# Kernel optimization log

Hardware: AMD Instinct MI355X
Metric: run time of the kernel (lower is better)

Reference implementation:

```python
import jax, jax.numpy as jnp
import numpy as np

B, S, H, U = 32, 2048, 1024, 1024


def setup_inputs() -> dict:
    key = jax.random.key(0)
    ks = jax.random.split(key, 8)
    sH = 1.0 / np.sqrt(H)
    sU = 1.0 / np.sqrt(U)
    return {
        "encoder_output": jax.random.normal(ks[0], (B, S, H), dtype=jnp.float32),
        "last_layer_h_n": jax.random.normal(ks[1], (B, H), dtype=jnp.float32),
        # torch Linear stores weight [out,in]; we store transposed [in,out] for x @ W
        "W1_w": jax.random.uniform(ks[2], (H, U), jnp.float32, -sH, sH),
        "W1_b": jax.random.uniform(ks[3], (U,), jnp.float32, -sH, sH),
        "W2_w": jax.random.uniform(ks[4], (H, U), jnp.float32, -sH, sH),
        "W2_b": jax.random.uniform(ks[5], (U,), jnp.float32, -sH, sH),
        "V_w": jax.random.uniform(ks[6], (U, 1), jnp.float32, -sU, sU),
        "V_b": jax.random.uniform(ks[7], (1,), jnp.float32, -sU, sU),
    }


def reference(encoder_output, last_layer_h_n, W1_w, W1_b, W2_w, W2_b, V_w, V_b):
    # proj_enc: [B,S,U]; proj_h: [B,1,U] (unsqueeze(1) broadcast)
    proj_enc = jnp.einsum("bsh,hu->bsu", encoder_output, W1_w) + W1_b
    proj_h = (last_layer_h_n @ W2_w + W2_b)[:, None, :]
    # score: [B,S,1]
    score = jnp.tanh(proj_enc + proj_h) @ V_w + V_b
    # softmax over the sequence axis (dim 1)
    attention_weights = jax.nn.softmax(score, axis=1)
    # NOTE: in the original module context_vector is always None (dead branch),
    # so the faithful output is attention_weights alone.
    return attention_weights
```

## Files before the change

### kernel.cpp

```cpp
#include <hip/hip_runtime.h>
#include <hip/hip_bf16.h>


typedef __bf16 bf16x8 __attribute__((ext_vector_type(8)));
typedef float  f32x4  __attribute__((ext_vector_type(4)));

#define HDIM 1024
#define UDIM 1024
#define SDIM 2048
#define MROWS 65536
#define BM 128
#define BN 128
#define BK 32

__device__ inline unsigned short f2bf(float x) {
    return __builtin_bit_cast(unsigned short, (__bf16)x);
}

__device__ inline float fast_tanh(float x) {
    float z = __expf(-2.0f * __builtin_fabsf(x));
    float t = __fdividef(1.0f - z, 1.0f + z);
    return __builtin_copysignf(t, x);
}

#define GLDS16(gp, lp)                                                              \
    __builtin_amdgcn_global_load_lds(                                               \
        (const __attribute__((address_space(1))) unsigned int*)(gp),                \
        (__attribute__((address_space(3))) unsigned int*)(lp), 16, 0, 0)

__global__ __launch_bounds__(256) void cvt_kernel(const float* __restrict__ in,
                                                  unsigned short* __restrict__ out) {
    size_t i = ((size_t)blockIdx.x * 256 + threadIdx.x) * 8;
    const float4 f0 = *(const float4*)(in + i);
    const float4 f1 = *(const float4*)(in + i + 4);
    ushort4 h0, h1;
    h0.x = f2bf(f0.x); h0.y = f2bf(f0.y); h0.z = f2bf(f0.z); h0.w = f2bf(f0.w);
    h1.x = f2bf(f1.x); h1.y = f2bf(f1.y); h1.z = f2bf(f1.z); h1.w = f2bf(f1.w);
    *(ushort4*)(out + i) = h0;
    *(ushort4*)(out + i + 4) = h1;
}

__global__ void w1t_kernel(const float* __restrict__ W1, unsigned short* __restrict__ W1T) {
    __shared__ float tile[32][33];
    int bx = blockIdx.x;
    int by = blockIdx.y;
    int tx = threadIdx.x, ty = threadIdx.y;
#pragma unroll
    for (int r = 0; r < 4; ++r) {
        int h = by * 32 + ty + r * 8;
        int u = bx * 32 + tx;
        tile[ty + r * 8][tx] = W1[h * UDIM + u];
    }
    __syncthreads();
#pragma unroll
    for (int r = 0; r < 4; ++r) {
        int u = bx * 32 + ty + r * 8;
        int h = by * 32 + tx;
        W1T[u * HDIM + h] = f2bf(tile[tx][ty + r * 8]);
    }
}

__global__ void php_kernel(const float* __restrict__ hn, const float* __restrict__ W2,
                           float* __restrict__ php) {
    int u = (blockIdx.x & 3) * 256 + threadIdx.x;
    int b = blockIdx.y;
    int hc = blockIdx.z;
    int h0 = hc * 128;
    float acc = 0.f;
#pragma unroll 8
    for (int h = h0; h < h0 + 128; ++h)
        acc = fmaf(hn[b * HDIM + h], W2[h * UDIM + u], acc);
    php[(hc * 32 + b) * UDIM + u] = acc;
}

__global__ void ph_combine(const float* __restrict__ php, const float* __restrict__ W1b,
                           const float* __restrict__ W2b, float* __restrict__ ph) {
    int idx = blockIdx.x * 256 + threadIdx.x;
    int u = idx & (UDIM - 1);
    int b = idx >> 10;
    float acc = W1b[u] + W2b[u];
#pragma unroll
    for (int p = 0; p < 8; ++p) acc += php[(p * 32 + b) * UDIM + u];
    ph[idx] = acc;
}

__global__ __launch_bounds__(256) void score_kernel(
    const unsigned short* __restrict__ encb, const unsigned short* __restrict__ W1T,
    const float* __restrict__ ph, const float* __restrict__ Vw,
    float* __restrict__ part) {
    __shared__ unsigned short As[BM * BK];
    __shared__ unsigned short Bs[BN * BK];

    const int bx = blockIdx.x;
    const int x = bx & 7;
    const int k = bx >> 3;
    const int tile_n = k & 7;
    const int tile_m = (x << 6) | (k >> 3);

    const int t = threadIdx.x;
    const int lane = t & 63;
    const int wid = t >> 6;
    const int wm = wid >> 1, wn = wid & 1;

    const int row0 = tile_m * BM;
    const int col0 = tile_n * BN;

    f32x4 acc[4][4];
#pragma unroll
    for (int i = 0; i < 4; ++i)
#pragma unroll
        for (int j = 0; j < 4; ++j)
            acc[i][j] = (f32x4){0.f, 0.f, 0.f, 0.f};

    const int mrow = lane & 15;
    const int kq = (lane >> 4) * 8;

    const int c0 = wid * 64 + lane;
    const int c1 = c0 + 256;
    const unsigned ldsA0 = (unsigned)(wid * 64) * 16;
    const unsigned ldsA1 = ldsA0 + 256 * 16;

    for (int kt = 0; kt < HDIM; kt += BK) {
        {
            const unsigned short* ga0 = encb + (size_t)(row0 + (c0 >> 2)) * HDIM + kt + (c0 & 3) * 8;
            const unsigned short* ga1 = encb + (size_t)(row0 + (c1 >> 2)) * HDIM + kt + (c1 & 3) * 8;
            const unsigned short* gb0 = W1T + (size_t)(col0 + (c0 >> 2)) * HDIM + kt + (c0 & 3) * 8;
            const unsigned short* gb1 = W1T + (size_t)(col0 + (c1 >> 2)) * HDIM + kt + (c1 & 3) * 8;
            GLDS16(ga0, (char*)As + ldsA0);
            GLDS16(ga1, (char*)As + ldsA1);
            GLDS16(gb0, (char*)Bs + ldsA0);
            GLDS16(gb1, (char*)Bs + ldsA1);
        }
        __syncthreads();

        bf16x8 a[4], bb[4];
#pragma unroll
        for (int i = 0; i < 4; ++i)
            a[i] = *reinterpret_cast<const bf16x8*>(As + (wm * 64 + i * 16 + mrow) * BK + kq);
#pragma unroll
        for (int j = 0; j < 4; ++j)
            bb[j] = *reinterpret_cast<const bf16x8*>(Bs + (wn * 64 + j * 16 + mrow) * BK + kq);
#pragma unroll
        for (int i = 0; i < 4; ++i)
#pragma unroll
            for (int j = 0; j < 4; ++j)
                acc[i][j] = __builtin_amdgcn_mfma_f32_16x16x32_bf16(a[i], bb[j], acc[i][j], 0, 0, 0);
        __syncthreads();
    }

    const int b = row0 >> 11;
    const int colg = lane & 15;
    const int rowq = (lane >> 4) * 4;
    float vw[4], phv[4];
#pragma unroll
    for (int j = 0; j < 4; ++j) {
        int u = col0 + wn * 64 + j * 16 + colg;
        vw[j] = Vw[u];
        phv[j] = ph[b * UDIM + u];
    }
#pragma unroll
    for (int i = 0; i < 4; ++i) {
#pragma unroll
        for (int r = 0; r < 4; ++r) {
            float s = 0.f;
#pragma unroll
            for (int j = 0; j < 4; ++j) {
                float pe = acc[i][j][r] + phv[j];
                s += fast_tanh(pe) * vw[j];
            }
            s += __shfl_xor(s, 1);
            s += __shfl_xor(s, 2);
            s += __shfl_xor(s, 4);
            s += __shfl_xor(s, 8);
            if (colg == 0) {
                int row = row0 + wm * 64 + i * 16 + rowq + r;
                part[(size_t)(tile_n * 2 + wn) * MROWS + row] = s;
            }
        }
    }
}

#define LDK 40
__global__ __launch_bounds__(256) void score_kernel_f32(
    const float* __restrict__ enc, const unsigned short* __restrict__ W1T,
    const float* __restrict__ ph, const float* __restrict__ Vw,
    float* __restrict__ part) {
    __shared__ unsigned short As[BM * LDK];
    __shared__ unsigned short Bs[BN * LDK];

    const int bx = blockIdx.x;
    const int tile_n = bx & 7;
    const int tile_m = bx >> 3;
    const int t = threadIdx.x;
    const int lane = t & 63;
    const int wid = t >> 6;
    const int wm = wid >> 1, wn = wid & 1;

    const int row0 = tile_m * BM;
    const int col0 = tile_n * BN;

    f32x4 acc[4][4];
#pragma unroll
    for (int i = 0; i < 4; ++i)
#pragma unroll
        for (int j = 0; j < 4; ++j)
            acc[i][j] = (f32x4){0.f, 0.f, 0.f, 0.f};

    const int mrow = lane & 15;
    const int kq = (lane >> 4) * 8;

    for (int kt = 0; kt < HDIM; kt += BK) {
        __syncthreads();
#pragma unroll
        for (int i = 0; i < 4; ++i) {
            int c = t + 256 * i;
            int r = c >> 3;
            int kc = (c & 7) * 4;
            const float4 f = *(const float4*)(enc + (size_t)(row0 + r) * HDIM + kt + kc);
            ushort4 h;
            h.x = f2bf(f.x); h.y = f2bf(f.y); h.z = f2bf(f.z); h.w = f2bf(f.w);
            *(ushort4*)(As + r * LDK + kc) = h;
        }
#pragma unroll
        for (int i = 0; i < 2; ++i) {
            int c = t + 256 * i;
            int r = c >> 2;
            int kc = (c & 3) * 8;
            const uint4 v = *(const uint4*)(W1T + (size_t)(col0 + r) * HDIM + kt + kc);
            *(uint4*)(Bs + r * LDK + kc) = v;
        }
        __syncthreads();

        bf16x8 a[4], bb[4];
#pragma unroll
        for (int i = 0; i < 4; ++i)
            a[i] = *reinterpret_cast<const bf16x8*>(As + (wm * 64 + i * 16 + mrow) * LDK + kq);
#pragma unroll
        for (int j = 0; j < 4; ++j)
            bb[j] = *reinterpret_cast<const bf16x8*>(Bs + (wn * 64 + j * 16 + mrow) * LDK + kq);
#pragma unroll
        for (int i = 0; i < 4; ++i)
#pragma unroll
            for (int j = 0; j < 4; ++j)
                acc[i][j] = __builtin_amdgcn_mfma_f32_16x16x32_bf16(a[i], bb[j], acc[i][j], 0, 0, 0);
    }

    const int b = row0 >> 11;
    const int colg = lane & 15;
    const int rowq = (lane >> 4) * 4;
    float vw[4], phv[4];
#pragma unroll
    for (int j = 0; j < 4; ++j) {
        int u = col0 + wn * 64 + j * 16 + colg;
        vw[j] = Vw[u];
        phv[j] = ph[b * UDIM + u];
    }
#pragma unroll
    for (int i = 0; i < 4; ++i) {
#pragma unroll
        for (int r = 0; r < 4; ++r) {
            float s = 0.f;
#pragma unroll
            for (int j = 0; j < 4; ++j) {
                float pe = acc[i][j][r] + phv[j];
                s += fast_tanh(pe) * vw[j];
            }
            s += __shfl_xor(s, 1);
            s += __shfl_xor(s, 2);
            s += __shfl_xor(s, 4);
            s += __shfl_xor(s, 8);
            if (colg == 0) {
                int row = row0 + wm * 64 + i * 16 + rowq + r;
                part[(size_t)(tile_n * 2 + wn) * MROWS + row] = s;
            }
        }
    }
}

__global__ void softmax_kernel(const float* __restrict__ part, float* __restrict__ out) {
    int b = blockIdx.x;
    int t = threadIdx.x;
    __shared__ float sred[4];
    float v[8];
    float lmax = -3.4e38f;
#pragma unroll
    for (int i = 0; i < 8; ++i) {
        int s = t + i * 256;
        float sum = 0.f;
#pragma unroll
        for (int p = 0; p < 16; ++p) sum += part[(size_t)p * MROWS + b * SDIM + s];
        v[i] = sum;
        lmax = fmaxf(lmax, sum);
    }
#pragma unroll
    for (int off = 1; off < 64; off <<= 1) lmax = fmaxf(lmax, __shfl_xor(lmax, off));
    if ((t & 63) == 0) sred[t >> 6] = lmax;
    __syncthreads();
    float bmax = fmaxf(fmaxf(sred[0], sred[1]), fmaxf(sred[2], sred[3]));
    __syncthreads();
    float lsum = 0.f;
#pragma unroll
    for (int i = 0; i < 8; ++i) {
        v[i] = expf(v[i] - bmax);
        lsum += v[i];
    }
#pragma unroll
    for (int off = 1; off < 64; off <<= 1) lsum += __shfl_xor(lsum, off);
    if ((t & 63) == 0) sred[t >> 6] = lsum;
    __syncthreads();
    float inv = 1.0f / (sred[0] + sred[1] + sred[2] + sred[3]);
#pragma unroll
    for (int i = 0; i < 8; ++i) out[b * SDIM + t + i * 256] = v[i] * inv;
}

extern "C" void kernel_launch(void* const* d_in, const int* in_sizes, int n_in,
                              void* d_out, int out_size, void* d_ws, size_t ws_size,
                              hipStream_t stream) {
    const float* enc = (const float*)d_in[0];
    const float* hn  = (const float*)d_in[1];
    const float* W1  = (const float*)d_in[2];
    const float* W1b = (const float*)d_in[3];
    const float* W2  = (const float*)d_in[4];
    const float* W2b = (const float*)d_in[5];
    const float* Vw  = (const float*)d_in[6];
    float* out = (float*)d_out;

    char* ws = (char*)d_ws;
    const size_t ENCB_BYTES = (size_t)MROWS * HDIM * 2;
    const size_t NEED = ENCB_BYTES + (2u << 20) + (128u << 10) + (1u << 20) + (4u << 20);

    if (ws_size >= NEED) {
        unsigned short* encb = (unsigned short*)ws;
        unsigned short* W1T  = (unsigned short*)(ws + ENCB_BYTES);
        float* ph   = (float*)(ws + ENCB_BYTES + (2u << 20));
        float* php  = (float*)(ws + ENCB_BYTES + (2u << 20) + (128u << 10));
        float* part = (float*)(ws + ENCB_BYTES + (2u << 20) + (128u << 10) + (1u << 20));

        cvt_kernel<<<32768, 256, 0, stream>>>(enc, encb);
        w1t_kernel<<<dim3(32, 32), dim3(32, 8), 0, stream>>>(W1, W1T);
        php_kernel<<<dim3(4, 32, 8), 256, 0, stream>>>(hn, W2, php);
        ph_combine<<<128, 256, 0, stream>>>(php, W1b, W2b, ph);
        score_kernel<<<dim3(4096), 256, 0, stream>>>(encb, W1T, ph, Vw, part);
        softmax_kernel<<<32, 256, 0, stream>>>(part, out);
    } else {
        unsigned short* W1T = (unsigned short*)ws;
        float* ph   = (float*)(ws + (2u << 20));
        float* php  = (float*)(ws + (2u << 20) + (128u << 10));
        float* part = (float*)(ws + (2u << 20) + (128u << 10) + (1u << 20));

        w1t_kernel<<<dim3(32, 32), dim3(32, 8), 0, stream>>>(W1, W1T);
        php_kernel<<<dim3(4, 32, 8), 256, 0, stream>>>(hn, W2, php);
        ph_combine<<<128, 256, 0, stream>>>(php, W1b, W2b, ph);
        score_kernel_f32<<<dim3(4096), 256, 0, stream>>>(enc, W1T, ph, Vw, part);
        softmax_kernel<<<32, 256, 0, stream>>>(part, out);
    }
}
```

Before: 596.4 us.

## Double K-tile depth and XOR-swizzle LDS layout in bf16 score GEMM

Raises the K step of the main bf16 GEMM kernel from 32 to 64, so each iteration issues four global-to-LDS loads per operand and runs two MFMA sub-steps, halving the number of barrier pairs. The LDS layout is XOR-swizzled on 16-byte chunks by row, so the fragment reads no longer hit the same banks. The fp32 fallback kernel keeps a 32-wide K step through a new FBK constant. The cost is twice the LDS footprint per block, which may lower occupancy.

```diff
diff --git a/kernel.cpp b/kernel.cpp
--- a/kernel.cpp
+++ b/kernel.cpp
@@ -11,7 +11,7 @@
 #define MROWS 65536
 #define BM 128
 #define BN 128
-#define BK 32
+#define BK 64
 
 __device__ inline unsigned short f2bf(float x) {
     return __builtin_bit_cast(unsigned short, (__bf16)x);
@@ -113,38 +113,47 @@
             acc[i][j] = (f32x4){0.f, 0.f, 0.f, 0.f};
 
     const int mrow = lane & 15;
-    const int kq = (lane >> 4) * 8;
-
-    const int c0 = wid * 64 + lane;
-    const int c1 = c0 + 256;
-    const unsigned ldsA0 = (unsigned)(wid * 64) * 16;
-    const unsigned ldsA1 = ldsA0 + 256 * 16;
+    const int swz = mrow & 7;
+    const int kgrp = lane >> 4;
+
+    const int cI = wid * 64 + lane;
+    int rS[4], klS[4];
+#pragma unroll
+    for (int issue = 0; issue < 4; ++issue) {
+        int c = cI + issue * 256;
+        rS[issue] = c >> 3;
+        klS[issue] = ((c & 7) ^ ((c >> 3) & 7)) * 8;
+    }
 
     for (int kt = 0; kt < HDIM; kt += BK) {
-        {
-            const unsigned short* ga0 = encb + (size_t)(row0 + (c0 >> 2)) * HDIM + kt + (c0 & 3) * 8;
-            const unsigned short* ga1 = encb + (size_t)(row0 + (c1 >> 2)) * HDIM + kt + (c1 & 3) * 8;
-            const unsigned short* gb0 = W1T + (size_t)(col0 + (c0 >> 2)) * HDIM + kt + (c0 & 3) * 8;
-            const unsigned short* gb1 = W1T + (size_t)(col0 + (c1 >> 2)) * HDIM + kt + (c1 & 3) * 8;
-            GLDS16(ga0, (char*)As + ldsA0);
-            GLDS16(ga1, (char*)As + ldsA1);
-            GLDS16(gb0, (char*)Bs + ldsA0);
-            GLDS16(gb1, (char*)Bs + ldsA1);
+#pragma unroll
+        for (int issue = 0; issue < 4; ++issue) {
+            const unsigned short* ga = encb + (size_t)(row0 + rS[issue]) * HDIM + kt + klS[issue];
+            GLDS16(ga, (char*)As + (unsigned)(issue * 256 + wid * 64) * 16);
+        }
+#pragma unroll
+        for (int issue = 0; issue < 4; ++issue) {
+            const unsigned short* gb = W1T + (size_t)(col0 + rS[issue]) * HDIM + kt + klS[issue];
+            GLDS16(gb, (char*)Bs + (unsigned)(issue * 256 + wid * 64) * 16);
         }
         __syncthreads();
 
-        bf16x8 a[4], bb[4];
-#pragma unroll
-        for (int i = 0; i < 4; ++i)
-            a[i] = *reinterpret_cast<const bf16x8*>(As + (wm * 64 + i * 16 + mrow) * BK + kq);
-#pragma unroll
-        for (int j = 0; j < 4; ++j)
-            bb[j] = *reinterpret_cast<const bf16x8*>(Bs + (wn * 64 + j * 16 + mrow) * BK + kq);
-#pragma unroll
-        for (int i = 0; i < 4; ++i)
+#pragma unroll
+        for (int s = 0; s < 2; ++s) {
+            const int phys = ((s * 4 + kgrp) ^ swz) * 8;
+            bf16x8 a[4], bb[4];
+#pragma unroll
+            for (int i = 0; i < 4; ++i)
+                a[i] = *reinterpret_cast<const bf16x8*>(As + (wm * 64 + i * 16 + mrow) * BK + phys);
 #pragma unroll
             for (int j = 0; j < 4; ++j)
-                acc[i][j] = __builtin_amdgcn_mfma_f32_16x16x32_bf16(a[i], bb[j], acc[i][j], 0, 0, 0);
+                bb[j] = *reinterpret_cast<const bf16x8*>(Bs + (wn * 64 + j * 16 + mrow) * BK + phys);
+#pragma unroll
+            for (int i = 0; i < 4; ++i)
+#pragma unroll
+                for (int j = 0; j < 4; ++j)
+                    acc[i][j] = __builtin_amdgcn_mfma_f32_16x16x32_bf16(a[i], bb[j], acc[i][j], 0, 0, 0);
+        }
         __syncthreads();
     }
 
@@ -181,6 +190,7 @@
 }
 
 #define LDK 40
+#define FBK 32
 __global__ __launch_bounds__(256) void score_kernel_f32(
     const float* __restrict__ enc, const unsigned short* __restrict__ W1T,
     const float* __restrict__ ph, const float* __restrict__ Vw,
@@ -209,7 +219,7 @@
     const int mrow = lane & 15;
     const int kq = (lane >> 4) * 8;
 
-    for (int kt = 0; kt < HDIM; kt += BK) {
+    for (int kt = 0; kt < HDIM; kt += FBK) {
         __syncthreads();
 #pragma unroll
         for (int i = 0; i < 4; ++i) {
```

After: 625.0 us. 4.8% more time.
